# Performance work log

Hardware: AMD Instinct MI355X
Metric: run time of the kernel (lower is better)

The kernel has to match this reference:

```python
import jax, jax.numpy as jnp
import numpy as np

B, L, HID, H = 2, 2048, 1024, 16
HD = HID // H
MAX_REL = 2


def setup_inputs() -> dict:
    key = jax.random.key(0)
    ks = jax.random.split(key, 16)
    s = 0.02
    return {
        "query": jax.random.normal(ks[0], (B, L, HID), jnp.float32),
        "key": jax.random.normal(ks[1], (B, L, HID), jnp.float32),
        "value": jax.random.normal(ks[2], (B, L, HID), jnp.float32),
        "Wq": jax.random.normal(ks[3], (HID, HID), jnp.float32) * s,
        "bq": jnp.zeros((HID,), jnp.float32),
        "Wk": jax.random.normal(ks[4], (HID, HID), jnp.float32) * s,
        "bk": jnp.zeros((HID,), jnp.float32),
        "Wv": jax.random.normal(ks[5], (HID, HID), jnp.float32) * s,
        "bv": jnp.zeros((HID,), jnp.float32),
        "Wo": jax.random.normal(ks[6], (HID, HID), jnp.float32) * s,
        "bo": jnp.zeros((HID,), jnp.float32),
        "rel_k_table": jax.random.normal(ks[7], (2 * MAX_REL + 1, HD), jnp.float32) * s,
        "rel_v_table": jax.random.normal(ks[8], (2 * MAX_REL + 1, HD), jnp.float32) * s,
    }


def _rel_embeddings(table, len_q, len_k):
    # Shaw-style clipped relative position lookup -> [len_q, len_k, head_dim]
    dist = jnp.arange(len_k)[None, :] - jnp.arange(len_q)[:, None]
    idx = jnp.clip(dist, -MAX_REL, MAX_REL) + MAX_REL
    return table[idx]


def reference(query, key, value, Wq, bq, Wk, bk, Wv, bv, Wo, bo, rel_k_table, rel_v_table):
    b, lq, hid = query.shape
    lk = key.shape[1]
    q = (query @ Wq.T + bq).reshape(b, lq, H, HD)   # [b, lq, h, hd]
    k = (key @ Wk.T + bk).reshape(b, lk, H, HD)     # [b, lk, h, hd]
    v = (value @ Wv.T + bv).reshape(b, lk, H, HD)   # [b, lk, h, hd]

    rk = _rel_embeddings(rel_k_table, lq, lk)       # [lq, lk, hd]
    rv = _rel_embeddings(rel_v_table, lq, lk)       # [lq, lk, hd]

    attn1 = jnp.einsum('bqhd,bkhd->bhqk', q, k)
    attn2 = jnp.einsum('bqhd,qkd->bhqk', q, rk)
    # NOTE: original code averages the two scores and does NOT divide by sqrt(head_dim)
    attn = jax.nn.softmax((attn1 + attn2) * 0.5, axis=-1)

    w1 = jnp.einsum('bhqk,bkhd->bhqd', attn, v)
    w2 = jnp.einsum('bhqk,qkd->bhqd', attn, rv)
    x = (w1 + w2).transpose(0, 2, 1, 3).reshape(b, lq, hid)
    return x @ Wo.T + bo
```

## Files before the change

### kernel.cpp

```cpp
#include <hip/hip_runtime.h>
#include <hip/hip_bf16.h>
#include <math.h>

typedef __attribute__((ext_vector_type(8))) short bf16x8;
typedef __attribute__((ext_vector_type(4))) float f32x4;
typedef __attribute__((ext_vector_type(16))) float f32x16;

constexpr int Bc   = 2;
constexpr int Lc   = 2048;
constexpr int HIDc = 1024;
constexpr int Hc   = 16;
constexpr int HDc  = 64;
constexpr int Mc   = 4096;

__device__ __forceinline__ ushort f2bf(float f) {
  uint u = __float_as_uint(f);
  u += 0x7fff + ((u >> 16) & 1);
  return (ushort)(u >> 16);
}

__device__ __forceinline__ void gload16(const ushort* g, ushort* l) {
  __builtin_amdgcn_global_load_lds(
      (const __attribute__((address_space(1))) uint*)(const void*)g,
      (__attribute__((address_space(3))) uint*)(void*)l, 16, 0, 0);
}

__device__ __forceinline__ uint cvtpk(float lo, float hi_) {
  uint r;
  asm("v_cvt_pk_bf16_f32 %0, %1, %2" : "=v"(r) : "v"(lo), "v"(hi_));
  return r;
}
__device__ __forceinline__ void pswap(uint &a, uint &b) {
  asm("v_permlane32_swap_b32 %0, %1" : "+v"(a), "+v"(b));
}

__global__ __launch_bounds__(256)
void cvt7(const float* __restrict__ q, const float* __restrict__ k,
          const float* __restrict__ v, const float* __restrict__ wq,
          const float* __restrict__ wk, const float* __restrict__ wv,
          const float* __restrict__ wo,
          ushort* dq_, ushort* dk, ushort* dv,
          ushort* dwq, ushort* dwk, ushort* dwv, ushort* dwo)
{
  int blk = blockIdx.x;
  const float* s; ushort* d; int off;
  if      (blk < 2048) { s = q;  d = dq_; off = blk; }
  else if (blk < 4096) { s = k;  d = dk;  off = blk - 2048; }
  else if (blk < 6144) { s = v;  d = dv;  off = blk - 4096; }
  else if (blk < 6656) { s = wq; d = dwq; off = blk - 6144; }
  else if (blk < 7168) { s = wk; d = dwk; off = blk - 6656; }
  else if (blk < 7680) { s = wv; d = dwv; off = blk - 7168; }
  else                 { s = wo; d = dwo; off = blk - 7680; }
  size_t i = (size_t)off * 2048 + threadIdx.x * 8;
  float4 a = *(const float4*)(s + i);
  float4 b = *(const float4*)(s + i + 4);
  ushort t[8] = { f2bf(a.x), f2bf(a.y), f2bf(a.z), f2bf(a.w),
                  f2bf(b.x), f2bf(b.y), f2bf(b.z), f2bf(b.w) };
  *(uint4*)(d + i) = *(uint4*)t;
}

__global__ __launch_bounds__(512)
void gemm_bf16(const ushort* __restrict__ A, const ushort* __restrict__ Bw,
               const float* __restrict__ bias, float* __restrict__ Cf,
               ushort* __restrict__ Cb, int M, int N, int K, int mode)
{
  __shared__ ushort As[2][128*32];
  __shared__ ushort Bs[2][128*32];
  const int tid  = threadIdx.x;
  const int lane = tid & 63;
  const int w    = tid >> 6;
  const int g    = lane >> 4;
  const int lc   = lane & 15;
  const int wr   = w >> 2;
  const int wc   = w & 3;
  const int row0 = blockIdx.y * 128;
  const int col0 = blockIdx.x * 128;

  const int sr  = tid >> 2;
  const int sc_ = tid & 3;
  const int scg = sc_ ^ ((sr >> 1) & 3);
  const ushort* pA = A  + (size_t)(row0 + sr) * K + scg * 8;
  const ushort* pB = Bw + (size_t)(col0 + sr) * K + scg * 8;

  int aoff[4], boff[2];
  #pragma unroll
  for (int mi = 0; mi < 4; ++mi) {
    int r = wr*64 + mi*16 + lc;
    aoff[mi] = r*32 + (g ^ ((r >> 1) & 3)) * 8;
  }
  #pragma unroll
  for (int ni = 0; ni < 2; ++ni) {
    int r = wc*32 + ni*16 + lc;
    boff[ni] = r*32 + (g ^ ((r >> 1) & 3)) * 8;
  }

  f32x4 acc[4][2];
  #pragma unroll
  for (int mi = 0; mi < 4; ++mi)
    #pragma unroll
    for (int ni = 0; ni < 2; ++ni) acc[mi][ni] = (f32x4){0.f,0.f,0.f,0.f};

  gload16(pA, &As[0][tid*8]);
  gload16(pB, &Bs[0][tid*8]);
  __syncthreads();

  const int NT = K >> 5;
  for (int t = 0; t < NT; ++t) {
    if (t + 1 < NT) {
      int k0 = (t + 1) << 5;
      gload16(pA + k0, &As[(t+1)&1][tid*8]);
      gload16(pB + k0, &Bs[(t+1)&1][tid*8]);
    }
    const ushort* as = As[t & 1];
    const ushort* bs = Bs[t & 1];
    bf16x8 af[4], bfr[2];
    #pragma unroll
    for (int mi = 0; mi < 4; ++mi) af[mi] = *(const bf16x8*)&as[aoff[mi]];
    #pragma unroll
    for (int ni = 0; ni < 2; ++ni) bfr[ni] = *(const bf16x8*)&bs[boff[ni]];
    #pragma unroll
    for (int mi = 0; mi < 4; ++mi)
      #pragma unroll
      for (int ni = 0; ni < 2; ++ni)
        acc[mi][ni] = __builtin_amdgcn_mfma_f32_16x16x32_bf16(af[mi], bfr[ni], acc[mi][ni], 0, 0, 0);
    __syncthreads();
  }

  const int colbase = col0 + wc*32;
  if (mode == 0) {
    #pragma unroll
    for (int mi = 0; mi < 4; ++mi) {
      int row = row0 + wr*64 + mi*16 + 4*g;
      #pragma unroll
      for (int ni = 0; ni < 2; ++ni) {
        int col = colbase + ni*16 + lc;
        float bb = bias[col];
        #pragma unroll
        for (int reg = 0; reg < 4; ++reg)
          Cf[(size_t)(row + reg) * N + col] = acc[mi][ni][reg] + bb;
      }
    }
  } else if (mode == 1) {
    #pragma unroll
    for (int mi = 0; mi < 4; ++mi) {
      int row = row0 + wr*64 + mi*16 + 4*g;
      int b = row >> 11, qq = row & 2047;
      #pragma unroll
      for (int ni = 0; ni < 2; ++ni) {
        int col = colbase + ni*16 + lc;
        int h = col >> 6, d = col & 63;
        float bb = bias[col];
        size_t base = (((size_t)b*Hc + h)*Lc + qq)*HDc + d;
        #pragma unroll
        for (int reg = 0; reg < 4; ++reg)
          Cb[base + (size_t)reg*HDc] = f2bf(acc[mi][ni][reg] + bb);
      }
    }
  } else {
    #pragma unroll
    for (int mi = 0; mi < 4; ++mi) {
      int row = row0 + wr*64 + mi*16 + 4*g;
      int b = row >> 11, kk = row & 2047;
      #pragma unroll
      for (int ni = 0; ni < 2; ++ni) {
        int col = colbase + ni*16 + lc;
        int h = col >> 6, d = col & 63;
        float bb = bias[col];
        ushort t4[4];
        #pragma unroll
        for (int reg = 0; reg < 4; ++reg) t4[reg] = f2bf(acc[mi][ni][reg] + bb);
        *(uint2*)&Cb[(((size_t)b*Hc + h)*HDc + d)*Lc + kk] = *(uint2*)t4;
      }
    }
  }
}

__global__ __launch_bounds__(128)
void attn_mfma32(const ushort* __restrict__ Qc, const ushort* __restrict__ Kc,
                 const ushort* __restrict__ Vt, const float* __restrict__ relk,
                 const float* __restrict__ relv, ushort* __restrict__ X)
{
  __shared__ ushort KVs[2][9216];
  __shared__ float epi[2][6][32];

  const int tid  = threadIdx.x;
  const int w    = tid >> 6;
  const int lane = tid & 63;
  const int lq   = lane & 31;
  const int hi   = lane >> 5;

  const int swz  = (blockIdx.x & 7) * 128 + (blockIdx.x >> 3);
  const int qblk = swz & 31;
  const int bh   = swz >> 5;
  const int b    = bh >> 4;
  const int h    = bh & 15;
  const int qw   = qblk*64 + w*32;
  const int qabs = qw + lq;

  constexpr float C2 = 0.72134752f;

  const ushort* Kbh = Kc + (size_t)bh*Lc*HDc;
  const ushort* Vbh = Vt + (size_t)bh*HDc*Lc;

  bf16x8 qf[4];
  const ushort* qbase = Qc + ((size_t)bh*Lc + qabs)*HDc + 8*hi;
  #pragma unroll
  for (int s = 0; s < 4; ++s) qf[s] = *(const bf16x8*)(qbase + 16*s);

  f32x16 dc;
  #pragma unroll
  for (int i = 0; i < 16; ++i) dc[i] = 0.f;
  #pragma unroll
  for (int s = 0; s < 4; ++s) {
    union { ushort u[8]; bf16x8 v; } rf;
    #pragma unroll
    for (int j = 0; j < 8; ++j) rf.u[j] = 0;
    if (lq < 5) {
      #pragma unroll
      for (int j = 0; j < 8; ++j) rf.u[j] = f2bf(relk[lq*HDc + 16*s + 8*hi + j]);
    }
    dc = __builtin_amdgcn_mfma_f32_32x32x16_bf16(rf.v, qf[s], dc, 0, 0, 0);
  }
  float o0 = __shfl_xor(dc[0], 32), o1 = __shfl_xor(dc[1], 32),
        o2 = __shfl_xor(dc[2], 32), o3 = __shfl_xor(dc[3], 32);
  float dqh0, dqh1, dqh2, dqh3, dqh4;
  if (hi == 0) { dqh0 = dc[0]; dqh1 = dc[1]; dqh2 = dc[2]; dqh3 = dc[3]; dqh4 = o0; }
  else         { dqh0 = o0;    dqh1 = o1;    dqh2 = o2;    dqh3 = o3;    dqh4 = dc[0]; }
  dqh0 *= C2; dqh1 *= C2; dqh2 *= C2; dqh3 *= C2; dqh4 *= C2;

  f32x16 acc0, acc1;
  #pragma unroll
  for (int i = 0; i < 16; ++i) { acc0[i] = 0.f; acc1[i] = 0.f; }
  float lsum = 0.f, llo = 0.f, e1 = 0.f, e2 = 0.f, e3 = 0.f;

  auto stage = [&](ushort* dst, int k0) {
    #pragma unroll
    for (int i = 0; i < 9; ++i) {
      int c = i*128 + tid;
      if (c < 576) {
        int row = c/9, ch = c - row*9;
        gload16(Kbh + (size_t)(k0 + row)*HDc + ch*8, dst + c*8);
      } else {
        int cv = c - 576;
        int row = cv/9, ch = cv - row*9;
        gload16(Vbh + (size_t)row*Lc + k0 + ch*8, dst + c*8);
      }
    }
  };

  auto group = [&](const f32x16& c, int kb, const ushort* vb_, int g) {
    float p[16];
    const bool allhi = (kb >= qw + 33);
    const bool alllo = (kb + 33 <= qw);
    if (allhi | alllo) {
      const float dq = allhi ? dqh4 : dqh0;
      #pragma unroll
      for (int r = 0; r < 16; ++r)
        p[r] = __builtin_amdgcn_exp2f(__builtin_fmaf(c[r], C2, dq));
      float gs = (((p[0]+p[1]) + (p[2]+p[3])) + ((p[4]+p[5]) + (p[6]+p[7])))
               + (((p[8]+p[9]) + (p[10]+p[11])) + ((p[12]+p[13]) + (p[14]+p[15])));
      lsum += gs;
      if (alllo) llo += gs;
    } else {
      int bnum = kb + 4*hi - qabs;
      #pragma unroll
      for (int r = 0; r < 16; ++r) {
        int dist = bnum + ((r & 3) + 8*(r >> 2));
        float dq = dist <= -2 ? dqh0 : (dist >= 2 ? dqh4 :
                   (dist == -1 ? dqh1 : (dist == 0 ? dqh2 : dqh3)));
        float pp = __builtin_amdgcn_exp2f(__builtin_fmaf(c[r], C2, dq));
        p[r] = pp; lsum += pp;
        llo += (dist <= -2) ? pp : 0.f;
        e1  += (dist == -1) ? pp : 0.f;
        e2  += (dist == 0)  ? pp : 0.f;
        e3  += (dist == 1)  ? pp : 0.f;
      }
    }
    #pragma unroll
    for (int s2 = 0; s2 < 2; ++s2) {
      uint X0 = cvtpk(p[8*s2+0], p[8*s2+1]);
      uint X1 = cvtpk(p[8*s2+2], p[8*s2+3]);
      uint Y0 = cvtpk(p[8*s2+4], p[8*s2+5]);
      uint Y1 = cvtpk(p[8*s2+6], p[8*s2+7]);
      pswap(X0, Y0); pswap(X1, Y1);
      union { uint u[4]; bf16x8 v; } aw;
      aw.u[0] = X0; aw.u[1] = X1; aw.u[2] = Y0; aw.u[3] = Y1;
      bf16x8 vf0 = *(const bf16x8*)&vb_[(lq)     *72 + (4*g + 2*s2 + hi)*8];
      bf16x8 vf1 = *(const bf16x8*)&vb_[(32 + lq)*72 + (4*g + 2*s2 + hi)*8];
      __builtin_amdgcn_s_setprio(1);
      acc0 = __builtin_amdgcn_mfma_f32_32x32x16_bf16(aw.v, vf0, acc0, 0, 0, 0);
      acc1 = __builtin_amdgcn_mfma_f32_32x32x16_bf16(aw.v, vf1, acc1, 0, 0, 0);
      __builtin_amdgcn_s_setprio(0);
    }
  };

  stage(KVs[0], 0);
  __syncthreads();

  for (int t = 0; t < Lc/64; ++t) {
    const ushort* kb_ = KVs[t & 1];
    const ushort* vb_ = kb_ + 4608;
    if (t + 1 < Lc/64) stage(KVs[(t+1) & 1], (t+1)*64);
    const int k0 = t*64;

    bf16x8 kfa[4], kfb[4];
    #pragma unroll
    for (int s = 0; s < 4; ++s) {
      kfa[s] = *(const bf16x8*)&kb_[(lq)     *72 + (hi + 2*s)*8];
      kfb[s] = *(const bf16x8*)&kb_[(32 + lq)*72 + (hi + 2*s)*8];
    }
    f32x16 c0, c1;
    #pragma unroll
    for (int i = 0; i < 16; ++i) { c0[i] = 0.f; c1[i] = 0.f; }
    __builtin_amdgcn_s_setprio(1);
    #pragma unroll
    for (int s = 0; s < 4; ++s)
      c0 = __builtin_amdgcn_mfma_f32_32x32x16_bf16(kfa[s], qf[s], c0, 0, 0, 0);
    #pragma unroll
    for (int s = 0; s < 4; ++s)
      c1 = __builtin_amdgcn_mfma_f32_32x32x16_bf16(kfb[s], qf[s], c1, 0, 0, 0);
    __builtin_amdgcn_s_setprio(0);

    group(c0, k0,      vb_, 0);
    group(c1, k0 + 32, vb_, 1);
    __syncthreads();
  }

  float Ls = lsum + __shfl_xor(lsum, 32);
  float Lo = llo  + __shfl_xor(llo, 32);
  float E1 = e1   + __shfl_xor(e1, 32);
  float E2 = e2   + __shfl_xor(e2, 32);
  float E3 = e3   + __shfl_xor(e3, 32);
  float inv = 1.f / Ls;
  float s0 = Lo*inv, s1_ = E1*inv, s2_ = E2*inv, s3_ = E3*inv;
  float s4_ = 1.f - s0 - s1_ - s2_ - s3_;
  if (lane < 32) {
    epi[w][0][lq] = inv; epi[w][1][lq] = s0;  epi[w][2][lq] = s1_;
    epi[w][3][lq] = s2_; epi[w][4][lq] = s3_; epi[w][5][lq] = s4_;
  }
  float rvv[5][2];
  #pragma unroll
  for (int r = 0; r < 5; ++r) {
    rvv[r][0] = relv[r*HDc + lq];
    rvv[r][1] = relv[r*HDc + 32 + lq];
  }
  asm volatile("s_waitcnt lgkmcnt(0)" ::: "memory");
  #pragma unroll
  for (int r = 0; r < 16; ++r) {
    int qloc = ((r & 3) + 8*(r >> 2)) + 4*hi;
    float iv = epi[w][0][qloc], t0 = epi[w][1][qloc], t1 = epi[w][2][qloc],
          t2 = epi[w][3][qloc], t3 = epi[w][4][qloc], t4 = epi[w][5][qloc];
    size_t rowb = ((size_t)b*Lc + qw + qloc)*HIDc + h*HDc;
    float v0 = acc0[r]*iv + t0*rvv[0][0] + t1*rvv[1][0] + t2*rvv[2][0]
             + t3*rvv[3][0] + t4*rvv[4][0];
    float v1 = acc1[r]*iv + t0*rvv[0][1] + t1*rvv[1][1] + t2*rvv[2][1]
             + t3*rvv[3][1] + t4*rvv[4][1];
    X[rowb + lq]      = f2bf(v0);
    X[rowb + 32 + lq] = f2bf(v1);
  }
}

extern "C" void kernel_launch(void* const* d_in, const int* in_sizes, int n_in,
                              void* d_out, int out_size, void* d_ws, size_t ws_size,
                              hipStream_t stream) {
  const float* query = (const float*)d_in[0];
  const float* key   = (const float*)d_in[1];
  const float* value = (const float*)d_in[2];
  const float* Wq    = (const float*)d_in[3];
  const float* bq    = (const float*)d_in[4];
  const float* Wk    = (const float*)d_in[5];
  const float* bk    = (const float*)d_in[6];
  const float* Wv    = (const float*)d_in[7];
  const float* bv    = (const float*)d_in[8];
  const float* Wo    = (const float*)d_in[9];
  const float* bo    = (const float*)d_in[10];
  const float* relk  = (const float*)d_in[11];
  const float* relv  = (const float*)d_in[12];
  float* out = (float*)d_out;

  size_t S2 = (size_t)Mc * HIDc;
  ushort* base = (ushort*)d_ws;
  ushort* R0 = base;
  ushort* R1 = base + S2;
  ushort* R2 = base + 2*S2;
  ushort* R3 = base + 3*S2;
  ushort* R4 = base + 4*S2;
  ushort* W5 = base + 5*S2;
  ushort* WqB = W5, *WkB = W5 + S2/4, *WvB = W5 + 2*(S2/4), *WoB = W5 + 3*(S2/4);

  cvt7<<<8192, 256, 0, stream>>>(query, key, value, Wq, Wk, Wv, Wo,
                                 R0, R1, R2, WqB, WkB, WvB, WoB);

  dim3 grid_g(HIDc / 128, Mc / 128);
  gemm_bf16<<<grid_g, 512, 0, stream>>>(R1, WkB, bk, nullptr, R3, Mc, HIDc, HIDc, 1);
  gemm_bf16<<<grid_g, 512, 0, stream>>>(R0, WqB, bq, nullptr, R1, Mc, HIDc, HIDc, 1);
  gemm_bf16<<<grid_g, 512, 0, stream>>>(R2, WvB, bv, nullptr, R4, Mc, HIDc, HIDc, 2);

  attn_mfma32<<<Bc * Hc * (Lc / 64), 128, 0, stream>>>(R1, R3, R4, relk, relv, R0);

  gemm_bf16<<<grid_g, 512, 0, stream>>>(R0, WoB, bo, out, nullptr, Mc, HIDc, HIDc, 0);
}
```

Before: 175.9 us.

## Fuse fp32-to-bf16 conversion into GEMMs, merge QKV launches, retile attention loop

Removes the separate conversion kernel. The GEMMs now load fp32 operands directly and convert them to bf16 while writing to shared memory, using 64x128 tiles. The three QKV projections become one launch, and the attention output stays fp32. The attention kernel moves from 64-key to 32-key tiles with smaller swizzled LDS staging, an occupancy hint, and a shuffle-based epilogue in place of the LDS one. This drops a full pass over the activations and weights, but the GEMMs lose async global-to-LDS loads and redo the weight conversion in every tile.

```diff
diff --git a/kernel.cpp b/kernel.cpp
--- a/kernel.cpp
+++ b/kernel.cpp
@@ -34,38 +34,13 @@
   asm("v_permlane32_swap_b32 %0, %1" : "+v"(a), "+v"(b));
 }
 
-__global__ __launch_bounds__(256)
-void cvt7(const float* __restrict__ q, const float* __restrict__ k,
-          const float* __restrict__ v, const float* __restrict__ wq,
-          const float* __restrict__ wk, const float* __restrict__ wv,
-          const float* __restrict__ wo,
-          ushort* dq_, ushort* dk, ushort* dv,
-          ushort* dwq, ushort* dwk, ushort* dwv, ushort* dwo)
+template<int MODE>
+__device__ __forceinline__ void gemm_core(
+    const float* __restrict__ A, const float* __restrict__ Bw,
+    const float* __restrict__ bias, float* __restrict__ Cf,
+    ushort* __restrict__ Cb, int tile,
+    ushort (*As)[2048], ushort (*Bs)[4096])
 {
-  int blk = blockIdx.x;
-  const float* s; ushort* d; int off;
-  if      (blk < 2048) { s = q;  d = dq_; off = blk; }
-  else if (blk < 4096) { s = k;  d = dk;  off = blk - 2048; }
-  else if (blk < 6144) { s = v;  d = dv;  off = blk - 4096; }
-  else if (blk < 6656) { s = wq; d = dwq; off = blk - 6144; }
-  else if (blk < 7168) { s = wk; d = dwk; off = blk - 6656; }
-  else if (blk < 7680) { s = wv; d = dwv; off = blk - 7168; }
-  else                 { s = wo; d = dwo; off = blk - 7680; }
-  size_t i = (size_t)off * 2048 + threadIdx.x * 8;
-  float4 a = *(const float4*)(s + i);
-  float4 b = *(const float4*)(s + i + 4);
-  ushort t[8] = { f2bf(a.x), f2bf(a.y), f2bf(a.z), f2bf(a.w),
-                  f2bf(b.x), f2bf(b.y), f2bf(b.z), f2bf(b.w) };
-  *(uint4*)(d + i) = *(uint4*)t;
-}
-
-__global__ __launch_bounds__(512)
-void gemm_bf16(const ushort* __restrict__ A, const ushort* __restrict__ Bw,
-               const float* __restrict__ bias, float* __restrict__ Cf,
-               ushort* __restrict__ Cb, int M, int N, int K, int mode)
-{
-  __shared__ ushort As[2][128*32];
-  __shared__ ushort Bs[2][128*32];
   const int tid  = threadIdx.x;
   const int lane = tid & 63;
   const int w    = tid >> 6;
@@ -73,19 +48,19 @@
   const int lc   = lane & 15;
   const int wr   = w >> 2;
   const int wc   = w & 3;
-  const int row0 = blockIdx.y * 128;
-  const int col0 = blockIdx.x * 128;
+  const int row0 = (tile >> 3) * 64;
+  const int col0 = (tile & 7) * 128;
 
   const int sr  = tid >> 2;
   const int sc_ = tid & 3;
-  const int scg = sc_ ^ ((sr >> 1) & 3);
-  const ushort* pA = A  + (size_t)(row0 + sr) * K + scg * 8;
-  const ushort* pB = Bw + (size_t)(col0 + sr) * K + scg * 8;
-
-  int aoff[4], boff[2];
-  #pragma unroll
-  for (int mi = 0; mi < 4; ++mi) {
-    int r = wr*64 + mi*16 + lc;
+  const int wofs = sr*32 + (sc_ ^ ((sr >> 1) & 3))*8;
+  const float* pA = A  + (size_t)(row0 + sr) * HIDc + sc_*8;
+  const float* pB = Bw + (size_t)(col0 + sr) * HIDc + sc_*8;
+
+  int aoff[2], boff[2];
+  #pragma unroll
+  for (int mi = 0; mi < 2; ++mi) {
+    int r = wr*32 + mi*16 + lc;
     aoff[mi] = r*32 + (g ^ ((r >> 1) & 3)) * 8;
   }
   #pragma unroll
@@ -94,56 +69,71 @@
     boff[ni] = r*32 + (g ^ ((r >> 1) & 3)) * 8;
   }
 
-  f32x4 acc[4][2];
-  #pragma unroll
-  for (int mi = 0; mi < 4; ++mi)
+  f32x4 acc[2][2];
+  #pragma unroll
+  for (int mi = 0; mi < 2; ++mi)
     #pragma unroll
     for (int ni = 0; ni < 2; ++ni) acc[mi][ni] = (f32x4){0.f,0.f,0.f,0.f};
 
-  gload16(pA, &As[0][tid*8]);
-  gload16(pB, &Bs[0][tid*8]);
+  float4 a0, a1, b0, b1;
+  auto ld = [&](int ko) {
+    b0 = *(const float4*)(pB + ko);
+    b1 = *(const float4*)(pB + ko + 4);
+    if (tid < 256) {
+      a0 = *(const float4*)(pA + ko);
+      a1 = *(const float4*)(pA + ko + 4);
+    }
+  };
+  auto wrbuf = [&](int bi) {
+    ushort tb[8] = { f2bf(b0.x), f2bf(b0.y), f2bf(b0.z), f2bf(b0.w),
+                     f2bf(b1.x), f2bf(b1.y), f2bf(b1.z), f2bf(b1.w) };
+    *(uint4*)&Bs[bi][wofs] = *(uint4*)tb;
+    if (tid < 256) {
+      ushort ta[8] = { f2bf(a0.x), f2bf(a0.y), f2bf(a0.z), f2bf(a0.w),
+                       f2bf(a1.x), f2bf(a1.y), f2bf(a1.z), f2bf(a1.w) };
+      *(uint4*)&As[bi][wofs] = *(uint4*)ta;
+    }
+  };
+
+  ld(0); wrbuf(0);
   __syncthreads();
 
-  const int NT = K >> 5;
-  for (int t = 0; t < NT; ++t) {
-    if (t + 1 < NT) {
-      int k0 = (t + 1) << 5;
-      gload16(pA + k0, &As[(t+1)&1][tid*8]);
-      gload16(pB + k0, &Bs[(t+1)&1][tid*8]);
-    }
+  for (int t = 0; t < 32; ++t) {
+    if (t < 31) ld((t + 1) * 32);
     const ushort* as = As[t & 1];
     const ushort* bs = Bs[t & 1];
-    bf16x8 af[4], bfr[2];
-    #pragma unroll
-    for (int mi = 0; mi < 4; ++mi) af[mi] = *(const bf16x8*)&as[aoff[mi]];
+    bf16x8 af[2], bfr[2];
+    #pragma unroll
+    for (int mi = 0; mi < 2; ++mi) af[mi] = *(const bf16x8*)&as[aoff[mi]];
     #pragma unroll
     for (int ni = 0; ni < 2; ++ni) bfr[ni] = *(const bf16x8*)&bs[boff[ni]];
     #pragma unroll
-    for (int mi = 0; mi < 4; ++mi)
+    for (int mi = 0; mi < 2; ++mi)
       #pragma unroll
       for (int ni = 0; ni < 2; ++ni)
         acc[mi][ni] = __builtin_amdgcn_mfma_f32_16x16x32_bf16(af[mi], bfr[ni], acc[mi][ni], 0, 0, 0);
+    if (t < 31) wrbuf((t + 1) & 1);
     __syncthreads();
   }
 
   const int colbase = col0 + wc*32;
-  if (mode == 0) {
-    #pragma unroll
-    for (int mi = 0; mi < 4; ++mi) {
-      int row = row0 + wr*64 + mi*16 + 4*g;
+  if (MODE == 0) {
+    #pragma unroll
+    for (int mi = 0; mi < 2; ++mi) {
+      int row = row0 + wr*32 + mi*16 + 4*g;
       #pragma unroll
       for (int ni = 0; ni < 2; ++ni) {
         int col = colbase + ni*16 + lc;
         float bb = bias[col];
         #pragma unroll
         for (int reg = 0; reg < 4; ++reg)
-          Cf[(size_t)(row + reg) * N + col] = acc[mi][ni][reg] + bb;
-      }
-    }
-  } else if (mode == 1) {
-    #pragma unroll
-    for (int mi = 0; mi < 4; ++mi) {
-      int row = row0 + wr*64 + mi*16 + 4*g;
+          Cf[(size_t)(row + reg) * HIDc + col] = acc[mi][ni][reg] + bb;
+      }
+    }
+  } else if (MODE == 1) {
+    #pragma unroll
+    for (int mi = 0; mi < 2; ++mi) {
+      int row = row0 + wr*32 + mi*16 + 4*g;
       int b = row >> 11, qq = row & 2047;
       #pragma unroll
       for (int ni = 0; ni < 2; ++ni) {
@@ -158,8 +148,8 @@
     }
   } else {
     #pragma unroll
-    for (int mi = 0; mi < 4; ++mi) {
-      int row = row0 + wr*64 + mi*16 + 4*g;
+    for (int mi = 0; mi < 2; ++mi) {
+      int row = row0 + wr*32 + mi*16 + 4*g;
       int b = row >> 11, kk = row & 2047;
       #pragma unroll
       for (int ni = 0; ni < 2; ++ni) {
@@ -175,13 +165,39 @@
   }
 }
 
-__global__ __launch_bounds__(128)
+__global__ __launch_bounds__(512)
+void gemm_fused(const float* __restrict__ q, const float* __restrict__ k,
+                const float* __restrict__ v,
+                const float* __restrict__ Wq, const float* __restrict__ Wk,
+                const float* __restrict__ Wv,
+                const float* __restrict__ bq, const float* __restrict__ bk,
+                const float* __restrict__ bv,
+                ushort* Qc, ushort* Kc, ushort* Vt)
+{
+  __shared__ ushort As[2][2048];
+  __shared__ ushort Bs[2][4096];
+  int gi   = blockIdx.x >> 9;
+  int tile = blockIdx.x & 511;
+  if (gi == 0)      gemm_core<1>(q, Wq, bq, nullptr, Qc, tile, As, Bs);
+  else if (gi == 1) gemm_core<1>(k, Wk, bk, nullptr, Kc, tile, As, Bs);
+  else              gemm_core<2>(v, Wv, bv, nullptr, Vt, tile, As, Bs);
+}
+
+__global__ __launch_bounds__(512)
+void gemm_out(const float* __restrict__ X, const float* __restrict__ Wo,
+              const float* __restrict__ bo, float* __restrict__ out)
+{
+  __shared__ ushort As[2][2048];
+  __shared__ ushort Bs[2][4096];
+  gemm_core<0>(X, Wo, bo, out, nullptr, blockIdx.x, As, Bs);
+}
+
+__global__ __launch_bounds__(128, 4)
 void attn_mfma32(const ushort* __restrict__ Qc, const ushort* __restrict__ Kc,
                  const ushort* __restrict__ Vt, const float* __restrict__ relk,
-                 const float* __restrict__ relv, ushort* __restrict__ X)
+                 const float* __restrict__ relv, float* __restrict__ X)
 {
-  __shared__ ushort KVs[2][9216];
-  __shared__ float epi[2][6][32];
+  __shared__ ushort KVs[2][4608];
 
   const int tid  = threadIdx.x;
   const int w    = tid >> 6;
@@ -235,94 +251,99 @@
 
   auto stage = [&](ushort* dst, int k0) {
     #pragma unroll
-    for (int i = 0; i < 9; ++i) {
-      int c = i*128 + tid;
-      if (c < 576) {
-        int row = c/9, ch = c - row*9;
-        gload16(Kbh + (size_t)(k0 + row)*HDc + ch*8, dst + c*8);
-      } else {
-        int cv = c - 576;
-        int row = cv/9, ch = cv - row*9;
-        gload16(Vbh + (size_t)row*Lc + k0 + ch*8, dst + c*8);
+    for (int seg = 0; seg < 5; ++seg) {
+      int widx = seg*2 + w;
+      if (widx < 5) {
+        int vc = widx*64 + lane;
+        int row = vc/5, ch = vc - row*5;
+        gload16(Vbh + (size_t)row*Lc + k0 + ch*8, dst + vc*8);
+      } else if (widx < 9) {
+        int kc = (widx - 5)*64 + lane;
+        int row = kc >> 3, pch = kc & 7;
+        int gch = pch ^ (row & 7);
+        gload16(Kbh + (size_t)(k0 + row)*HDc + gch*8, dst + (320 + kc)*8);
       }
     }
   };
 
-  auto group = [&](const f32x16& c, int kb, const ushort* vb_, int g) {
-    float p[16];
+  stage(KVs[0], 0);
+  __syncthreads();
+
+  for (int t = 0; t < Lc/32; ++t) {
+    const ushort* vb_ = KVs[t & 1];
+    const ushort* kb_ = vb_ + 2560;
+    if (t + 1 < Lc/32) stage(KVs[(t+1) & 1], (t+1)*32);
+    const int kb = t*32;
+
+    bf16x8 kfa[4];
+    #pragma unroll
+    for (int s = 0; s < 4; ++s)
+      kfa[s] = *(const bf16x8*)&kb_[lq*64 + ((2*s + hi) ^ (lq & 7))*8];
+    f32x16 c0;
+    #pragma unroll
+    for (int i = 0; i < 16; ++i) c0[i] = 0.f;
+    __builtin_amdgcn_s_setprio(1);
+    #pragma unroll
+    for (int s = 0; s < 4; ++s)
+      c0 = __builtin_amdgcn_mfma_f32_32x32x16_bf16(kfa[s], qf[s], c0, 0, 0, 0);
+    __builtin_amdgcn_s_setprio(0);
+
+    bf16x8 vf00 = *(const bf16x8*)&vb_[lq*40      + hi*8];
+    bf16x8 vf01 = *(const bf16x8*)&vb_[(32+lq)*40 + hi*8];
+    bf16x8 vf10 = *(const bf16x8*)&vb_[lq*40      + (2+hi)*8];
+    bf16x8 vf11 = *(const bf16x8*)&vb_[(32+lq)*40 + (2+hi)*8];
+
+    uint pk[8];
     const bool allhi = (kb >= qw + 33);
     const bool alllo = (kb + 33 <= qw);
     if (allhi | alllo) {
       const float dq = allhi ? dqh4 : dqh0;
-      #pragma unroll
-      for (int r = 0; r < 16; ++r)
-        p[r] = __builtin_amdgcn_exp2f(__builtin_fmaf(c[r], C2, dq));
-      float gs = (((p[0]+p[1]) + (p[2]+p[3])) + ((p[4]+p[5]) + (p[6]+p[7])))
-               + (((p[8]+p[9]) + (p[10]+p[11])) + ((p[12]+p[13]) + (p[14]+p[15])));
+      float gs = 0.f;
+      #pragma unroll
+      for (int jj = 0; jj < 8; ++jj) {
+        float pa = __builtin_amdgcn_exp2f(__builtin_fmaf(c0[2*jj],   C2, dq));
+        float pb = __builtin_amdgcn_exp2f(__builtin_fmaf(c0[2*jj+1], C2, dq));
+        gs += pa + pb;
+        pk[jj] = cvtpk(pa, pb);
+      }
       lsum += gs;
       if (alllo) llo += gs;
     } else {
       int bnum = kb + 4*hi - qabs;
       #pragma unroll
-      for (int r = 0; r < 16; ++r) {
-        int dist = bnum + ((r & 3) + 8*(r >> 2));
-        float dq = dist <= -2 ? dqh0 : (dist >= 2 ? dqh4 :
-                   (dist == -1 ? dqh1 : (dist == 0 ? dqh2 : dqh3)));
-        float pp = __builtin_amdgcn_exp2f(__builtin_fmaf(c[r], C2, dq));
-        p[r] = pp; lsum += pp;
-        llo += (dist <= -2) ? pp : 0.f;
-        e1  += (dist == -1) ? pp : 0.f;
-        e2  += (dist == 0)  ? pp : 0.f;
-        e3  += (dist == 1)  ? pp : 0.f;
-      }
-    }
-    #pragma unroll
-    for (int s2 = 0; s2 < 2; ++s2) {
-      uint X0 = cvtpk(p[8*s2+0], p[8*s2+1]);
-      uint X1 = cvtpk(p[8*s2+2], p[8*s2+3]);
-      uint Y0 = cvtpk(p[8*s2+4], p[8*s2+5]);
-      uint Y1 = cvtpk(p[8*s2+6], p[8*s2+7]);
-      pswap(X0, Y0); pswap(X1, Y1);
-      union { uint u[4]; bf16x8 v; } aw;
-      aw.u[0] = X0; aw.u[1] = X1; aw.u[2] = Y0; aw.u[3] = Y1;
-      bf16x8 vf0 = *(const bf16x8*)&vb_[(lq)     *72 + (4*g + 2*s2 + hi)*8];
-      bf16x8 vf1 = *(const bf16x8*)&vb_[(32 + lq)*72 + (4*g + 2*s2 + hi)*8];
-      __builtin_amdgcn_s_setprio(1);
-      acc0 = __builtin_amdgcn_mfma_f32_32x32x16_bf16(aw.v, vf0, acc0, 0, 0, 0);
-      acc1 = __builtin_amdgcn_mfma_f32_32x32x16_bf16(aw.v, vf1, acc1, 0, 0, 0);
-      __builtin_amdgcn_s_setprio(0);
-    }
-  };
-
-  stage(KVs[0], 0);
-  __syncthreads();
-
-  for (int t = 0; t < Lc/64; ++t) {
-    const ushort* kb_ = KVs[t & 1];
-    const ushort* vb_ = kb_ + 4608;
-    if (t + 1 < Lc/64) stage(KVs[(t+1) & 1], (t+1)*64);
-    const int k0 = t*64;
-
-    bf16x8 kfa[4], kfb[4];
-    #pragma unroll
-    for (int s = 0; s < 4; ++s) {
-      kfa[s] = *(const bf16x8*)&kb_[(lq)     *72 + (hi + 2*s)*8];
-      kfb[s] = *(const bf16x8*)&kb_[(32 + lq)*72 + (hi + 2*s)*8];
-    }
-    f32x16 c0, c1;
-    #pragma unroll
-    for (int i = 0; i < 16; ++i) { c0[i] = 0.f; c1[i] = 0.f; }
+      for (int jj = 0; jj < 8; ++jj) {
+        int r0 = 2*jj;
+        int d0 = bnum + ((r0 & 3) + 8*(r0 >> 2));
+        int d1 = d0 + 1;
+        float dqa = d0 <= -2 ? dqh0 : (d0 >= 2 ? dqh4 :
+                    (d0 == -1 ? dqh1 : (d0 == 0 ? dqh2 : dqh3)));
+        float dqb = d1 <= -2 ? dqh0 : (d1 >= 2 ? dqh4 :
+                    (d1 == -1 ? dqh1 : (d1 == 0 ? dqh2 : dqh3)));
+        float pa = __builtin_amdgcn_exp2f(__builtin_fmaf(c0[r0],   C2, dqa));
+        float pb = __builtin_amdgcn_exp2f(__builtin_fmaf(c0[r0+1], C2, dqb));
+        lsum += pa + pb;
+        llo += (d0 <= -2 ? pa : 0.f) + (d1 <= -2 ? pb : 0.f);
+        e1  += (d0 == -1 ? pa : 0.f) + (d1 == -1 ? pb : 0.f);
+        e2  += (d0 ==  0 ? pa : 0.f) + (d1 ==  0 ? pb : 0.f);
+        e3  += (d0 ==  1 ? pa : 0.f) + (d1 ==  1 ? pb : 0.f);
+        pk[jj] = cvtpk(pa, pb);
+      }
+    }
+
+    uint X0 = pk[0], X1 = pk[1], Y0 = pk[2], Y1 = pk[3];
+    pswap(X0, Y0); pswap(X1, Y1);
+    union { uint u[4]; bf16x8 v; } aw0;
+    aw0.u[0] = X0; aw0.u[1] = X1; aw0.u[2] = Y0; aw0.u[3] = Y1;
+    X0 = pk[4]; X1 = pk[5]; Y0 = pk[6]; Y1 = pk[7];
+    pswap(X0, Y0); pswap(X1, Y1);
+    union { uint u[4]; bf16x8 v; } aw1;
+    aw1.u[0] = X0; aw1.u[1] = X1; aw1.u[2] = Y0; aw1.u[3] = Y1;
     __builtin_amdgcn_s_setprio(1);
-    #pragma unroll
-    for (int s = 0; s < 4; ++s)
-      c0 = __builtin_amdgcn_mfma_f32_32x32x16_bf16(kfa[s], qf[s], c0, 0, 0, 0);
-    #pragma unroll
-    for (int s = 0; s < 4; ++s)
-      c1 = __builtin_amdgcn_mfma_f32_32x32x16_bf16(kfb[s], qf[s], c1, 0, 0, 0);
+    acc0 = __builtin_amdgcn_mfma_f32_32x32x16_bf16(aw0.v, vf00, acc0, 0, 0, 0);
+    acc1 = __builtin_amdgcn_mfma_f32_32x32x16_bf16(aw0.v, vf01, acc1, 0, 0, 0);
+    acc0 = __builtin_amdgcn_mfma_f32_32x32x16_bf16(aw1.v, vf10, acc0, 0, 0, 0);
+    acc1 = __builtin_amdgcn_mfma_f32_32x32x16_bf16(aw1.v, vf11, acc1, 0, 0, 0);
     __builtin_amdgcn_s_setprio(0);
-
-    group(c0, k0,      vb_, 0);
-    group(c1, k0 + 32, vb_, 1);
     __syncthreads();
   }
 
@@ -332,31 +353,29 @@
   float E2 = e2   + __shfl_xor(e2, 32);
   float E3 = e3   + __shfl_xor(e3, 32);
   float inv = 1.f / Ls;
-  float s0 = Lo*inv, s1_ = E1*inv, s2_ = E2*inv, s3_ = E3*inv;
-  float s4_ = 1.f - s0 - s1_ - s2_ - s3_;
-  if (lane < 32) {
-    epi[w][0][lq] = inv; epi[w][1][lq] = s0;  epi[w][2][lq] = s1_;
-    epi[w][3][lq] = s2_; epi[w][4][lq] = s3_; epi[w][5][lq] = s4_;
-  }
+  float s0v = Lo*inv, s1v = E1*inv, s2v = E2*inv, s3v = E3*inv;
+  float s4v = 1.f - s0v - s1v - s2v - s3v;
+
   float rvv[5][2];
   #pragma unroll
   for (int r = 0; r < 5; ++r) {
     rvv[r][0] = relv[r*HDc + lq];
     rvv[r][1] = relv[r*HDc + 32 + lq];
   }
-  asm volatile("s_waitcnt lgkmcnt(0)" ::: "memory");
   #pragma unroll
   for (int r = 0; r < 16; ++r) {
     int qloc = ((r & 3) + 8*(r >> 2)) + 4*hi;
-    float iv = epi[w][0][qloc], t0 = epi[w][1][qloc], t1 = epi[w][2][qloc],
-          t2 = epi[w][3][qloc], t3 = epi[w][4][qloc], t4 = epi[w][5][qloc];
-    size_t rowb = ((size_t)b*Lc + qw + qloc)*HIDc + h*HDc;
-    float v0 = acc0[r]*iv + t0*rvv[0][0] + t1*rvv[1][0] + t2*rvv[2][0]
-             + t3*rvv[3][0] + t4*rvv[4][0];
-    float v1 = acc1[r]*iv + t0*rvv[0][1] + t1*rvv[1][1] + t2*rvv[2][1]
-             + t3*rvv[3][1] + t4*rvv[4][1];
-    X[rowb + lq]      = f2bf(v0);
-    X[rowb + 32 + lq] = f2bf(v1);
+    float iv = __shfl(inv, qloc);
+    float t0 = __shfl(s0v, qloc);
+    float t1 = __shfl(s1v, qloc);
+    float t2 = __shfl(s2v, qloc);
+    float t3 = __shfl(s3v, qloc);
+    float t4 = __shfl(s4v, qloc);
+    size_t rowb = ((size_t)(b*Lc + qw + qloc))*HIDc + h*HDc;
+    X[rowb + lq]      = acc0[r]*iv + t0*rvv[0][0] + t1*rvv[1][0] + t2*rvv[2][0]
+                      + t3*rvv[3][0] + t4*rvv[4][0];
+    X[rowb + 32 + lq] = acc1[r]*iv + t0*rvv[0][1] + t1*rvv[1][1] + t2*rvv[2][1]
+                      + t3*rvv[3][1] + t4*rvv[4][1];
   }
 }
 
@@ -378,25 +397,16 @@
   const float* relv  = (const float*)d_in[12];
   float* out = (float*)d_out;
 
-  size_t S2 = (size_t)Mc * HIDc;
-  ushort* base = (ushort*)d_ws;
-  ushort* R0 = base;
-  ushort* R1 = base + S2;
-  ushort* R2 = base + 2*S2;
-  ushort* R3 = base + 3*S2;
-  ushort* R4 = base + 4*S2;
-  ushort* W5 = base + 5*S2;
-  ushort* WqB = W5, *WkB = W5 + S2/4, *WvB = W5 + 2*(S2/4), *WoB = W5 + 3*(S2/4);
-
-  cvt7<<<8192, 256, 0, stream>>>(query, key, value, Wq, Wk, Wv, Wo,
-                                 R0, R1, R2, WqB, WkB, WvB, WoB);
-
-  dim3 grid_g(HIDc / 128, Mc / 128);
-  gemm_bf16<<<grid_g, 512, 0, stream>>>(R1, WkB, bk, nullptr, R3, Mc, HIDc, HIDc, 1);
-  gemm_bf16<<<grid_g, 512, 0, stream>>>(R0, WqB, bq, nullptr, R1, Mc, HIDc, HIDc, 1);
-  gemm_bf16<<<grid_g, 512, 0, stream>>>(R2, WvB, bv, nullptr, R4, Mc, HIDc, HIDc, 2);
-
-  attn_mfma32<<<Bc * Hc * (Lc / 64), 128, 0, stream>>>(R1, R3, R4, relk, relv, R0);
-
-  gemm_bf16<<<grid_g, 512, 0, stream>>>(R0, WoB, bo, out, nullptr, Mc, HIDc, HIDc, 0);
-}
+  size_t S = (size_t)Bc * Hc * Lc * HDc;
+  ushort* Qc = (ushort*)d_ws;
+  ushort* Kc = Qc + S;
+  ushort* Vt = Kc + S;
+  float*  Xb = (float*)(Vt + S);
+
+  gemm_fused<<<3*512, 512, 0, stream>>>(query, key, value, Wq, Wk, Wv,
+                                        bq, bk, bv, Qc, Kc, Vt);
+
+  attn_mfma32<<<Bc * Hc * (Lc / 64), 128, 0, stream>>>(Qc, Kc, Vt, relk, relv, Xb);
+
+  gemm_out<<<512, 512, 0, stream>>>(Xb, Wo, bo, out);
+}
```

After: 270.3 us. 53.7% more time.
